# Kernel optimization log

Measured on AMD Instinct MI355X. Metric: run time of the kernel, lower is better.

## Reference

```python
import jax, jax.numpy as jnp
import numpy as np

MAXDISP = 192


def setup_inputs() -> dict:
    key = jax.random.key(0)
    k1, k2, k3 = jax.random.split(key, 3)
    B, C_color, D, H, W = 1, 3, MAXDISP, 192, 384
    # v: [B, 1 + C_color, D, H, W + D - 1]; channel 0 = matching cost ('block'), 1: = color
    v = jax.random.normal(k1, (B, 1 + C_color, D, H, W + D - 1), dtype=jnp.float32)
    x = jax.random.normal(k2, (B, C_color, H, W), dtype=jnp.float32)  # only supplies H, W
    y = jax.random.normal(k3, (B, C_color, H, W), dtype=jnp.float32)  # unused by forward
    return {"v": v, "x": x, "y": y}


def reference(v, x, y):
    D = MAXDISP
    B, _, H, W = x.shape
    block = v[:, 0:1]          # [B, 1, D, H, Wfull]
    color = v[:, 1:]           # [B, C, D, H, Wfull]

    # disparity values D-1 ... 0 along the disparity axis
    disp_vals = jnp.arange(D - 1, -1, -1, dtype=v.dtype).reshape(1, 1, D, 1, 1)

    # view 1: plain crop to width W
    block_1 = block[..., :W]
    color_1v = color[..., :W]
    w = jax.nn.softmax(block_1, axis=2)                 # softmax over disparity
    disp_1 = jnp.sum(w * disp_vals, axis=2)[:, 0]       # [B, H, W]
    color_1 = jnp.sum(w * color_1v, axis=2)             # [B, C, H, W]

    # view 2: per-disparity shifted crop. For disparity index d the shift is (D-1-d):
    #   out[..., d, :, w] = in[..., d, :, (D-1-d) + w]
    shift = (D - 1 - jnp.arange(D))[:, None] + jnp.arange(W)[None, :]   # [D, W]
    idx = shift.reshape(1, 1, D, 1, W)
    block_2 = jnp.take_along_axis(block, idx, axis=4)   # [B, 1, D, H, W]
    color_2v = jnp.take_along_axis(color, idx, axis=4)  # [B, C, D, H, W] (idx broadcasts)
    w2 = jax.nn.softmax(block_2, axis=2)
    disp_2 = jnp.sum(w2 * disp_vals, axis=2)[:, 0]      # [B, H, W]
    color_2 = jnp.sum(w2 * color_2v, axis=2)            # [B, C, H, W]

    return (color_1, color_2, disp_1, disp_2)
```

## Files before the change

### kernel.cpp

```cpp
#include <hip/hip_runtime.h>
#include <math.h>

#define DD 192
#define HH 192
#define WW 384
#define WV 575
#define PIX 32
#define NCHUNK 8
#define DPC 24

__global__ __launch_bounds__(256, 4) void vr_kernel(const float* __restrict__ v,
                                                    float* __restrict__ out) {
    const int t = threadIdx.x;
    const int wl = t & (PIX - 1);
    const int chunk = t >> 5;
    const int tile = blockIdx.x;
    const int h = tile / (WW / PIX);
    const int w0 = (tile % (WW / PIX)) * PIX;
    const int w = w0 + wl;

    const size_t dstride = (size_t)HH * WV;
    const size_t cstride = (size_t)DD * dstride;
    const float* base = v + (size_t)h * WV + (size_t)w;

    float m1 = -INFINITY, l1 = 0.f, a1 = 0.f, c10 = 0.f, c11 = 0.f, c12 = 0.f;
    float m2 = -INFINITY, l2 = 0.f, a2 = 0.f, c20 = 0.f, c21 = 0.f, c22 = 0.f;

    const int d0 = chunk * DPC;
    const float* p = base + (size_t)d0 * dstride;
    #pragma unroll 4
    for (int i = 0; i < DPC; ++i) {
        const int d = d0 + i;
        const int sh = (DD - 1) - d;
        float b1  = p[0];
        float b2  = p[sh];
        float x10 = p[cstride];
        float x20 = p[cstride + sh];
        float x11 = p[2 * cstride];
        float x21 = p[2 * cstride + sh];
        float x12 = p[3 * cstride];
        float x22 = p[3 * cstride + sh];
        const float dv = (float)sh;

        float nm = fmaxf(m1, b1);
        float s  = __expf(m1 - nm);
        float pr = __expf(b1 - nm);
        l1  = l1  * s + pr;
        a1  = a1  * s + pr * dv;
        c10 = c10 * s + pr * x10;
        c11 = c11 * s + pr * x11;
        c12 = c12 * s + pr * x12;
        m1 = nm;

        nm = fmaxf(m2, b2);
        s  = __expf(m2 - nm);
        pr = __expf(b2 - nm);
        l2  = l2  * s + pr;
        a2  = a2  * s + pr * dv;
        c20 = c20 * s + pr * x20;
        c21 = c21 * s + pr * x21;
        c22 = c22 * s + pr * x22;
        m2 = nm;

        p += dstride;
    }

    __shared__ float sm[NCHUNK][PIX][12];
    float* sp = sm[chunk][wl];
    sp[0] = m1; sp[1] = l1; sp[2]  = a1; sp[3]  = c10; sp[4]  = c11; sp[5]  = c12;
    sp[6] = m2; sp[7] = l2; sp[8]  = a2; sp[9]  = c20; sp[10] = c21; sp[11] = c22;
    __syncthreads();

    if (t < 2 * PIX) {
        const int pix  = t & (PIX - 1);
        const int pass = t >> 5;
        const int off  = pass * 6;
        float M = -INFINITY, L = 0.f, A = 0.f, C0 = 0.f, C1 = 0.f, C2 = 0.f;
        #pragma unroll
        for (int ch = 0; ch < NCHUNK; ++ch) {
            const float* q = sm[ch][pix] + off;
            float mm = q[0];
            float nm = fmaxf(M, mm);
            float s0 = __expf(M - nm);
            float s1 = __expf(mm - nm);
            L  = L  * s0 + q[1] * s1;
            A  = A  * s0 + q[2] * s1;
            C0 = C0 * s0 + q[3] * s1;
            C1 = C1 * s0 + q[4] * s1;
            C2 = C2 * s0 + q[5] * s1;
            M = nm;
        }
        const float inv = 1.0f / L;
        const int HW = HH * WW;
        const int o = h * WW + w0 + pix;
        out[(pass * 3 + 0) * HW + o] = C0 * inv;
        out[(pass * 3 + 1) * HW + o] = C1 * inv;
        out[(pass * 3 + 2) * HW + o] = C2 * inv;
        out[(6 + pass) * HW + o]     = A * inv;
    }
}

extern "C" void kernel_launch(void* const* d_in, const int* in_sizes, int n_in,
                              void* d_out, int out_size, void* d_ws, size_t ws_size,
                              hipStream_t stream) {
    const float* v = (const float*)d_in[0];
    float* out = (float*)d_out;
    const int grid = (HH * WW / PIX);
    vr_kernel<<<grid, 256, 0, stream>>>(v, out);
}
```

Measured before the change: 450.6 us.

## Stage full disparity rows in LDS and split merge into separate kernel

New measurement: 521.7 us. 15.8% more time.

```diff
diff --git a/kernel.cpp b/kernel.cpp
--- a/kernel.cpp
+++ b/kernel.cpp
@@ -5,41 +5,46 @@
 #define HH 192
 #define WW 384
 #define WV 575
-#define PIX 32
 #define NCHUNK 8
 #define DPC 24
+#define TPB 384
 
-__global__ __launch_bounds__(256, 4) void vr_kernel(const float* __restrict__ v,
-                                                    float* __restrict__ out) {
+__global__ __launch_bounds__(TPB, 8) void vr_partial(const float* __restrict__ v,
+                                                     float* __restrict__ ws) {
     const int t = threadIdx.x;
-    const int wl = t & (PIX - 1);
-    const int chunk = t >> 5;
-    const int tile = blockIdx.x;
-    const int h = tile / (WW / PIX);
-    const int w0 = (tile % (WW / PIX)) * PIX;
-    const int w = w0 + wl;
+    const int h = blockIdx.x >> 3;
+    const int chunk = blockIdx.x & 7;
+    const int d0 = chunk * DPC;
 
     const size_t dstride = (size_t)HH * WV;
     const size_t cstride = (size_t)DD * dstride;
-    const float* base = v + (size_t)h * WV + (size_t)w;
+
+    __shared__ float rows[4][WV + 1];
 
     float m1 = -INFINITY, l1 = 0.f, a1 = 0.f, c10 = 0.f, c11 = 0.f, c12 = 0.f;
     float m2 = -INFINITY, l2 = 0.f, a2 = 0.f, c20 = 0.f, c21 = 0.f, c22 = 0.f;
 
-    const int d0 = chunk * DPC;
-    const float* p = base + (size_t)d0 * dstride;
-    #pragma unroll 4
+    const float* rowbase = v + (size_t)h * WV + (size_t)d0 * dstride;
     for (int i = 0; i < DPC; ++i) {
         const int d = d0 + i;
         const int sh = (DD - 1) - d;
-        float b1  = p[0];
-        float b2  = p[sh];
-        float x10 = p[cstride];
-        float x20 = p[cstride + sh];
-        float x11 = p[2 * cstride];
-        float x21 = p[2 * cstride + sh];
-        float x12 = p[3 * cstride];
-        float x22 = p[3 * cstride + sh];
+        const float* r = rowbase + (size_t)i * dstride;
+        #pragma unroll
+        for (int c = 0; c < 4; ++c) {
+            const float* rc = r + (size_t)c * cstride;
+            rows[c][t] = rc[t];
+            if (t < WV - TPB) rows[c][t + TPB] = rc[t + TPB];
+        }
+        __syncthreads();
+
+        const float b1  = rows[0][t];
+        const float b2  = rows[0][t + sh];
+        const float x10 = rows[1][t];
+        const float x20 = rows[1][t + sh];
+        const float x11 = rows[2][t];
+        const float x21 = rows[2][t + sh];
+        const float x12 = rows[3][t];
+        const float x22 = rows[3][t + sh];
         const float dv = (float)sh;
 
         float nm = fmaxf(m1, b1);
@@ -62,37 +67,42 @@
         c22 = c22 * s + pr * x22;
         m2 = nm;
 
-        p += dstride;
+        __syncthreads();
     }
 
-    __shared__ float sm[NCHUNK][PIX][12];
-    float* sp = sm[chunk][wl];
-    sp[0] = m1; sp[1] = l1; sp[2]  = a1; sp[3]  = c10; sp[4]  = c11; sp[5]  = c12;
-    sp[6] = m2; sp[7] = l2; sp[8]  = a2; sp[9]  = c20; sp[10] = c21; sp[11] = c22;
-    __syncthreads();
+    float* wp = ws + (((size_t)h * NCHUNK + chunk) * 12) * WW + t;
+    wp[0 * WW] = m1;  wp[1 * WW] = l1;  wp[2 * WW]  = a1;
+    wp[3 * WW] = c10; wp[4 * WW] = c11; wp[5 * WW]  = c12;
+    wp[6 * WW] = m2;  wp[7 * WW] = l2;  wp[8 * WW]  = a2;
+    wp[9 * WW] = c20; wp[10 * WW] = c21; wp[11 * WW] = c22;
+}
 
-    if (t < 2 * PIX) {
-        const int pix  = t & (PIX - 1);
-        const int pass = t >> 5;
-        const int off  = pass * 6;
+__global__ __launch_bounds__(256, 4) void vr_merge(const float* __restrict__ ws,
+                                                   float* __restrict__ out) {
+    const int pix = blockIdx.x * 256 + threadIdx.x;
+    const int h = pix / WW;
+    const int w = pix - h * WW;
+    const int HW = HH * WW;
+
+    #pragma unroll
+    for (int pass = 0; pass < 2; ++pass) {
         float M = -INFINITY, L = 0.f, A = 0.f, C0 = 0.f, C1 = 0.f, C2 = 0.f;
         #pragma unroll
         for (int ch = 0; ch < NCHUNK; ++ch) {
-            const float* q = sm[ch][pix] + off;
-            float mm = q[0];
-            float nm = fmaxf(M, mm);
-            float s0 = __expf(M - nm);
-            float s1 = __expf(mm - nm);
-            L  = L  * s0 + q[1] * s1;
-            A  = A  * s0 + q[2] * s1;
-            C0 = C0 * s0 + q[3] * s1;
-            C1 = C1 * s0 + q[4] * s1;
-            C2 = C2 * s0 + q[5] * s1;
+            const float* q = ws + (((size_t)h * NCHUNK + ch) * 12 + pass * 6) * WW + w;
+            const float mm = q[0];
+            const float nm = fmaxf(M, mm);
+            const float s0 = __expf(M - nm);
+            const float s1 = __expf(mm - nm);
+            L  = L  * s0 + q[1 * WW] * s1;
+            A  = A  * s0 + q[2 * WW] * s1;
+            C0 = C0 * s0 + q[3 * WW] * s1;
+            C1 = C1 * s0 + q[4 * WW] * s1;
+            C2 = C2 * s0 + q[5 * WW] * s1;
             M = nm;
         }
         const float inv = 1.0f / L;
-        const int HW = HH * WW;
-        const int o = h * WW + w0 + pix;
+        const int o = h * WW + w;
         out[(pass * 3 + 0) * HW + o] = C0 * inv;
         out[(pass * 3 + 1) * HW + o] = C1 * inv;
         out[(pass * 3 + 2) * HW + o] = C2 * inv;
@@ -105,6 +115,7 @@
                               hipStream_t stream) {
     const float* v = (const float*)d_in[0];
     float* out = (float*)d_out;
-    const int grid = (HH * WW / PIX);
-    vr_kernel<<<grid, 256, 0, stream>>>(v, out);
+    float* ws = (float*)d_ws;
+    vr_partial<<<HH * NCHUNK, TPB, 0, stream>>>(v, ws);
+    vr_merge<<<(HH * WW) / 256, 256, 0, stream>>>(ws, out);
 }
```
